# Kernel tuning notes

Hardware: AMD Instinct MI355X
Metric: run time of the kernel (lower is better)

The kernel has to match this reference:

```python
import jax, jax.numpy as jnp
import numpy as np

B, H, S = 128, 256, 19
K0, D0 = 512, 32
K1, D1 = 512, 64
K2, D2 = 512, 64


def _conv(x, w, b):
    # 3x3 SAME conv, NCHW / OIHW
    y = jax.lax.conv_general_dilated(x, w, (1, 1), 'SAME',
                                     dimension_numbers=('NCHW', 'OIHW', 'NCHW'))
    return y + b[None, :, None, None]


def _bn(x, g, b, eps=1e-5):
    # BatchNorm2d in training mode: batch statistics over (N, H, W)
    m = x.mean((0, 2, 3), keepdims=True)
    v = x.var((0, 2, 3), keepdims=True)
    return g[None, :, None, None] * (x - m) * jax.lax.rsqrt(v + eps) + b[None, :, None, None]


def _vq(lat, E):
    # cdist^2 -> argmin -> gather, with straight-through gradient copy
    shp = lat.shape
    d = E.shape[1]
    lp = lat.reshape(-1, d)                                   # row-major flatten, as torch .view
    dist = (lp * lp).sum(-1, keepdims=True) + (E * E).sum(-1) - 2.0 * (lp @ E.T)
    k = jnp.argmin(dist, axis=-1)
    zd = E[k]
    zg = lp + jax.lax.stop_gradient(zd - lp)
    return k.reshape(shp[0], -1), zd.reshape(shp), zg.reshape(shp)


def setup_inputs() -> dict:
    key = jax.random.key(0)
    ks = iter(jax.random.split(key, 64))
    def rn(shape, s=0.02):
        return (s * jax.random.normal(next(ks), shape)).astype(jnp.float32)
    inp = {
        'observations': jax.random.normal(next(ks), (B, 18, S, S), jnp.float32),
        'hierarchy_usages': jax.random.uniform(next(ks), (B, 2), jnp.float32),
        'h0_conv_w': rn((H, 18, 3, 3), 0.05), 'h0_conv_b': jnp.zeros((H,)),
        'h0_bn_g': jnp.ones((H,)), 'h0_bn_b': jnp.zeros((H,)),
        'rb_c1_w': rn((3, H, H, 3, 3)), 'rb_c1_b': jnp.zeros((3, H)),
        'rb_bn1_g': jnp.ones((3, H)), 'rb_bn1_b': jnp.zeros((3, H)),
        'rb_c2_w': rn((3, H, H, 3, 3)), 'rb_c2_b': jnp.zeros((3, H)),
        'rb_bn2_g': jnp.ones((3, H)), 'rb_bn2_b': jnp.zeros((3, H)),
        'h0_conv2_w': rn((32, H, 3, 3)), 'h0_conv2_b': jnp.zeros((32,)),
        'h0_bn2_g': jnp.ones((32,)), 'h0_bn2_b': jnp.zeros((32,)),
        'E0': rn((K0, D0)), 'E1': rn((K1, D1)), 'E2': rn((K2, D2)),
        'h1_fc_w': rn((D0 * S * S, 256)), 'h1_fc_b': jnp.zeros((256,)),
        'h1_fc2_w': rn((256, D1 * 8)), 'h1_fc2_b': jnp.zeros((D1 * 8,)),
        'h2_fc_w': rn((D1 * 8, 128)), 'h2_fc_b': jnp.zeros((128,)),
        'h2_fc2_w': rn((128, D2 * 8)), 'h2_fc2_b': jnp.zeros((D2 * 8,)),
        'h2_fc3_w': rn((D2 * 8, 128)), 'h2_fc3_b': jnp.zeros((128,)),
        'h2_fc4_w': rn((128, D1 * 8)), 'h2_fc4_b': jnp.zeros((D1 * 8,)),
        'h1_fc3_w': rn((D1 * 8, 256)), 'h1_fc3_b': jnp.zeros((256,)),
        'h1_fc4_w': rn((256, D0 * S * S)), 'h1_fc4_b': jnp.zeros((D0 * S * S,)),
        'policy_w': rn((32 * S * S, 362)), 'policy_b': jnp.zeros((362,)),
        'value_w': rn((32 * S * S, 1)), 'value_b': jnp.zeros((1,)),
    }
    return inp


def _forward(observations, hierarchy_usages, h0_conv_w, h0_conv_b, h0_bn_g, h0_bn_b,
             rb_c1_w, rb_c1_b, rb_bn1_g, rb_bn1_b, rb_c2_w, rb_c2_b, rb_bn2_g, rb_bn2_b,
             h0_conv2_w, h0_conv2_b, h0_bn2_g, h0_bn2_b, E0, E1, E2,
             h1_fc_w, h1_fc_b, h1_fc2_w, h1_fc2_b, h2_fc_w, h2_fc_b, h2_fc2_w, h2_fc2_b,
             h2_fc3_w, h2_fc3_b, h2_fc4_w, h2_fc4_b, h1_fc3_w, h1_fc3_b, h1_fc4_w, h1_fc4_b,
             policy_w, policy_b, value_w, value_b):
    n = observations.shape[0]
    x = jax.nn.relu(_bn(_conv(observations, h0_conv_w, h0_conv_b), h0_bn_g, h0_bn_b))
    for i in range(3):
        xi = x
        x = jax.nn.relu(_bn(_conv(x, rb_c1_w[i], rb_c1_b[i]), rb_bn1_g[i], rb_bn1_b[i]))
        x = _bn(_conv(x, rb_c2_w[i], rb_c2_b[i]), rb_bn2_g[i], rb_bn2_b[i])
        x = jax.nn.relu(xi + x)
    x = jnp.tanh(_bn(_conv(x, h0_conv2_w, h0_conv2_b), h0_bn2_g, h0_bn2_b))  # [B,32,19,19]
    ze0 = x
    k0, zq0, zql0 = _vq(x, E0)
    em0 = jnp.broadcast_to(E0.mean(0)[None, :, None, None], (n, E0.shape[1], S, S))
    x = jax.lax.stop_gradient(x).reshape(-1, 32 * S * S)
    x = jax.nn.relu(x @ h1_fc_w + h1_fc_b)
    x = jnp.tanh(x @ h1_fc2_w + h1_fc2_b).reshape(-1, E1.shape[1], 8)
    ze1 = x
    k1, zq1, zql1 = _vq(x, E1)
    em1 = jnp.broadcast_to(E1.mean(0)[None, :, None], (n, E1.shape[1], 8))
    x = jax.lax.stop_gradient(x).reshape(-1, E1.shape[1] * 8)
    x = jax.nn.relu(x @ h2_fc_w + h2_fc_b)
    x = jnp.tanh(x @ h2_fc2_w + h2_fc2_b).reshape(-1, E2.shape[1], 8)
    ze2 = x
    k2, zq2, zql2 = _vq(x, E2)
    em2 = jnp.broadcast_to(E2.mean(0)[None, :, None], (n, E2.shape[1], 8))
    # top-down decoder path
    x = zql2.reshape(-1, E2.shape[1] * 8)
    x = jax.nn.relu(x @ h2_fc3_w + h2_fc3_b)
    x = jnp.tanh(x @ h2_fc4_w + h2_fc4_b).reshape(-1, E1.shape[1], 8)
    u1 = hierarchy_usages[:, 1][:, None, None]
    x = u1 * zql1 + (1.0 - u1) * x
    x = x.reshape(-1, E1.shape[1] * 8)
    x = jax.nn.relu(x @ h1_fc3_w + h1_fc3_b)
    x = jnp.tanh(x @ h1_fc4_w + h1_fc4_b).reshape(-1, E0.shape[1], S, S)
    u0 = hierarchy_usages[:, 0][:, None, None, None]
    x = u0 * zql0 + (1.0 - u0) * x
    x = x.reshape(-1, 32 * S * S)
    policy = x @ policy_w + policy_b
    value = jnp.tanh(x @ value_w + value_b)
    return (policy, value, ze0, ze1, ze2, zq0, zq1, zq2, k0, k1, k2,
            zql0, zql1, zql2, em0, em1, em2)


def reference(observations, hierarchy_usages, h0_conv_w, h0_conv_b, h0_bn_g, h0_bn_b,
              rb_c1_w, rb_c1_b, rb_bn1_g, rb_bn1_b, rb_c2_w, rb_c2_b, rb_bn2_g, rb_bn2_b,
              h0_conv2_w, h0_conv2_b, h0_bn2_g, h0_bn2_b, E0, E1, E2,
              h1_fc_w, h1_fc_b, h1_fc2_w, h1_fc2_b, h2_fc_w, h2_fc_b, h2_fc2_w, h2_fc2_b,
              h2_fc3_w, h2_fc3_b, h2_fc4_w, h2_fc4_b, h1_fc3_w, h1_fc3_b, h1_fc4_w, h1_fc4_b,
              policy_w, policy_b, value_w, value_b):
    return _forward(observations, hierarchy_usages, h0_conv_w, h0_conv_b, h0_bn_g, h0_bn_b,
                    rb_c1_w, rb_c1_b, rb_bn1_g, rb_bn1_b, rb_c2_w, rb_c2_b, rb_bn2_g, rb_bn2_b,
                    h0_conv2_w, h0_conv2_b, h0_bn2_g, h0_bn2_b, E0, E1, E2,
                    h1_fc_w, h1_fc_b, h1_fc2_w, h1_fc2_b, h2_fc_w, h2_fc_b, h2_fc2_w, h2_fc2_b,
                    h2_fc3_w, h2_fc3_b, h2_fc4_w, h2_fc4_b, h1_fc3_w, h1_fc3_b, h1_fc4_w, h1_fc4_b,
                    policy_w, policy_b, value_w, value_b)
```

## Files before the change

### kernel.cpp

```cpp
#include <hip/hip_runtime.h>
#include <hip/hip_bf16.h>

typedef long long i64;
typedef __attribute__((ext_vector_type(8))) short bf16x8;
typedef __attribute__((ext_vector_type(4))) float f32x4;

static constexpr i64 OUT_POLICY = 0;
static constexpr i64 OUT_VALUE  = 46336;
static constexpr i64 OUT_ZE0    = 46464;
static constexpr i64 OUT_ZE1    = 1525120;
static constexpr i64 OUT_ZE2    = 1590656;
static constexpr i64 OUT_ZQ0    = 1656192;
static constexpr i64 OUT_ZQ1    = 3134848;
static constexpr i64 OUT_ZQ2    = 3200384;
static constexpr i64 OUT_K0     = 3265920;
static constexpr i64 OUT_K1     = 3312128;
static constexpr i64 OUT_K2     = 3313152;
static constexpr i64 OUT_ZQL0   = 3314176;
static constexpr i64 OUT_ZQL1   = 4792832;
static constexpr i64 OUT_ZQL2   = 4858368;
static constexpr i64 OUT_EM0    = 4923904;
static constexpr i64 OUT_EM1    = 6402560;
static constexpr i64 OUT_EM2    = 6468096;
static constexpr i64 OUT_TOTAL  = 6533632;

__device__ __forceinline__ short bf16_hi(float v, float* back)
{
    unsigned b = __float_as_uint(v);
    unsigned hb = (b + 0x8000u) & 0xFFFF0000u;
    *back = __uint_as_float(hb);
    return (short)(hb >> 16);
}
__device__ __forceinline__ short bf16_of(float v)
{
    return (short)((__float_as_uint(v) + 0x8000u) >> 16);
}

__global__ void wtr_k(const float* __restrict__ w, float* __restrict__ wt,
                      int COUT, int CIN)
{
    int total = COUT * CIN * 9;
    for (int idx = blockIdx.x * blockDim.x + threadIdx.x; idx < total;
         idx += gridDim.x * blockDim.x) {
        int co = idx / (CIN * 9);
        int r  = idx - co * CIN * 9;
        int ci = r / 9;
        int tap = r - ci * 9;
        wt[((i64)tap * CIN + ci) * COUT + co] = w[idx];
    }
}

__global__ void wtr4_k(const float* __restrict__ w, short* __restrict__ wt4,
                       int CIN, int COUT)
{
    int NC = CIN / 32;
    int total = NC * 9 * 2 * 8192;
    for (int idx = blockIdx.x * blockDim.x + threadIdx.x; idx < total;
         idx += gridDim.x * blockDim.x) {
        int tile = idx >> 13;
        int pos  = idx & 8191;
        int row   = pos >> 6;
        int sslot = (pos >> 3) & 7;
        int r     = pos & 7;
        int slot  = sslot ^ (row & 7);
        int k2    = slot * 8 + r;
        int ct = tile & 1;
        int s  = tile >> 1;
        int c  = s / 9, t = s - c * 9;
        int co = ct * 128 + row;
        int ci = c * 32 + (k2 & 31);
        short outv = 0;
        if (co < COUT) {
            float v = w[((i64)co * CIN + ci) * 9 + t];
            float hf;
            short hs = bf16_hi(v, &hf);
            outv = (k2 < 32) ? hs : bf16_of(v - hf);
        }
        wt4[idx] = outv;
    }
}

template<int CIN>
__global__ __launch_bounds__(256)
void convmfma_k(const float* __restrict__ X, const short* __restrict__ WT4,
                float* __restrict__ Y, int coutT)
{
    constexpr int NC = CIN / 32;
    constexpr int NS = NC * 9;
    __shared__ short At[2][8192];
    __shared__ short Bt[2][8192];
    const int tid  = threadIdx.x;
    const int lane = tid & 63;
    const int w    = tid >> 6;
    const int wco  = (w & 1) * 64;
    const int wsp  = (w >> 1) * 64;
    const int col0 = blockIdx.x * 128;
    const int ct   = blockIdx.y;
    const int co0  = ct * 128;

    const int spS = tid & 127;
    const int cig = tid >> 7;
    const int colS = col0 + spS;
    const int nS = colS / 361;
    const int sS = colS - nS * 361;
    const int yS = sS / 19, xS = sS - yS * 19;
    const float* Xb = X + (i64)nS * CIN * 361 + sS;

    float xvP[16], xvQ[16];

#define BAR16 asm volatile("s_waitcnt vmcnt(16) lgkmcnt(0)\n\ts_barrier" ::: "memory")
#define BAR0  asm volatile("s_waitcnt vmcnt(0) lgkmcnt(0)\n\ts_barrier" ::: "memory")

#define A_ISSUE(BUF, S)                                                         \
    {                                                                           \
        const short* gp0 = WT4 + ((i64)((S) * 2 + ct) << 13) + (w << 11) + (lane << 3); \
        short* lp0 = &At[BUF][(w << 11)];                                       \
        __builtin_amdgcn_global_load_lds(gp0,        lp0,        16, 0, 0);     \
        __builtin_amdgcn_global_load_lds(gp0 + 512,  lp0 + 512,  16, 0, 0);     \
        __builtin_amdgcn_global_load_lds(gp0 + 1024, lp0 + 1024, 16, 0, 0);     \
        __builtin_amdgcn_global_load_lds(gp0 + 1536, lp0 + 1536, 16, 0, 0);     \
    }

#define B_LOAD(S, XV)                                                           \
    {                                                                           \
        const int c_ = (S) / 9, t_ = (S) - c_ * 9;                              \
        const int ky_ = t_ / 3, kx_ = t_ - ky_ * 3;                             \
        const bool v_ = (yS + ky_ >= 1) & (yS + ky_ <= 19) &                    \
                        (xS + kx_ >= 1) & (xS + kx_ <= 19);                     \
        const float* xp_ = Xb + (i64)(c_ * 32 + cig * 16) * 361                 \
                              + (ky_ - 1) * 19 + (kx_ - 1);                     \
        _Pragma("unroll")                                                       \
        for (int j = 0; j < 16; j++) XV[j] = v_ ? xp_[(i64)j * 361] : 0.f;      \
    }

#define B_WRITE(BUF, XV)                                                        \
    {                                                                           \
        bf16x8 h0, h1, l0, l1;                                                  \
        _Pragma("unroll")                                                       \
        for (int j = 0; j < 8; j++) {                                           \
            float hf;                                                           \
            short hs = bf16_hi(XV[j], &hf);                                     \
            h0[j] = hs; l0[j] = bf16_of(XV[j] - hf);                            \
        }                                                                       \
        _Pragma("unroll")                                                       \
        for (int j = 0; j < 8; j++) {                                           \
            float hf;                                                           \
            short hs = bf16_hi(XV[8 + j], &hf);                                 \
            h1[j] = hs; l1[j] = bf16_of(XV[8 + j] - hf);                        \
        }                                                                       \
        short* bp = &Bt[BUF][spS << 6];                                         \
        const int sw = spS & 7;                                                 \
        *(bf16x8*)(bp + (((cig * 2 + 0) ^ sw) << 3)) = h0;                      \
        *(bf16x8*)(bp + (((cig * 2 + 1) ^ sw) << 3)) = h1;                      \
        *(bf16x8*)(bp + (((4 + cig * 2 + 0) ^ sw) << 3)) = l0;                  \
        *(bf16x8*)(bp + (((4 + cig * 2 + 1) ^ sw) << 3)) = l1;                  \
    }

#define COMPUTE(CUR)                                                            \
    {                                                                           \
        bf16x8 bfr[2][4];                                                       \
        _Pragma("unroll")                                                       \
        for (int hb = 0; hb < 2; hb++)                                          \
            _Pragma("unroll")                                                   \
            for (int fb = 0; fb < 4; fb++) {                                    \
                int row = wsp + fb * 16 + (lane & 15);                          \
                int slot = hb * 4 + (lane >> 4);                                \
                bfr[hb][fb] = *(const bf16x8*)&Bt[CUR][(row << 6) + (((slot ^ (row & 7))) << 3)]; \
            }                                                                   \
        _Pragma("unroll")                                                       \
        for (int ha = 0; ha < 2; ha++)                                          \
            _Pragma("unroll")                                                   \
            for (int fa = 0; fa < 4; fa++) {                                    \
                int row = wco + fa * 16 + (lane & 15);                          \
                int slot = ha * 4 + (lane >> 4);                                \
                bf16x8 af = *(const bf16x8*)&At[CUR][(row << 6) + (((slot ^ (row & 7))) << 3)]; \
                _Pragma("unroll")                                               \
                for (int hb = 0; hb < 2; hb++)                                  \
                    _Pragma("unroll")                                           \
                    for (int fb = 0; fb < 4; fb++)                              \
                        acc[fa][fb] = __builtin_amdgcn_mfma_f32_16x16x32_bf16(  \
                            af, bfr[hb][fb], acc[fa][fb], 0, 0, 0);             \
            }                                                                   \
    }

#define ITER(S, XP, XN)                                                         \
    {                                                                           \
        if ((S) + 1 < NS) { BAR16; } else { BAR0; }                             \
        const int cur_ = ((S) & 1);                                             \
        if ((S) + 1 < NS) A_ISSUE(cur_ ^ 1, (S) + 1)                            \
        if ((S) + 2 < NS) B_LOAD((S) + 2, XN)                                   \
        COMPUTE(cur_)                                                           \
        if ((S) + 1 < NS) B_WRITE(cur_ ^ 1, XP)                                 \
    }

    f32x4 acc[4][4];
#pragma unroll
    for (int i = 0; i < 4; i++)
#pragma unroll
        for (int j = 0; j < 4; j++) acc[i][j] = (f32x4){0.f, 0.f, 0.f, 0.f};

    B_LOAD(0, xvP)
    B_WRITE(0, xvP)
    A_ISSUE(0, 0)
    B_LOAD(1, xvP)

    for (int s = 0; s < NS; s += 2) {
        ITER(s, xvP, xvQ)
        ITER(s + 1, xvQ, xvP)
    }
#undef BAR16
#undef BAR0
#undef A_ISSUE
#undef B_LOAD
#undef B_WRITE
#undef COMPUTE
#undef ITER

#pragma unroll
    for (int fb = 0; fb < 4; fb++) {
        int col = col0 + wsp + fb * 16 + (lane & 15);
        int nT = col / 361, sT = col - nT * 361;
        float* yp = Y + ((i64)nT * coutT + co0 + wco) * 361 + sT;
#pragma unroll
        for (int fa = 0; fa < 4; fa++)
#pragma unroll
            for (int r = 0; r < 4; r++) {
                int m = fa * 16 + (lane >> 4) * 4 + r;
                if (co0 + wco + m < coutT) yp[(i64)m * 361] = acc[fa][fb][r];
            }
    }
}

template<int CIN>
__global__ __launch_bounds__(256)
void convgemm_k(const float* __restrict__ X, const float* __restrict__ wt,
                float* __restrict__ Y, int wtW, int coW0, int coutT)
{
    constexpr int NCB = (CIN + 15) / 16;
    constexpr int NS  = 9 * NCB;
    __shared__ float Ws[2][16][128];
    __shared__ float Bs[2][16][128];
    const int tid  = threadIdx.x;
    const int col0 = blockIdx.x * 128;
    const int co0  = blockIdx.y * 128;
    const int tn = tid & 15;
    const int tm = (tid >> 4) & 15;
    const int kkS  = tid >> 5;
    const int cS0  = (tid & 31) * 4;

    int y_[4], x_[4];
    const float* Xb[4];
#pragma unroll
    for (int j = 0; j < 4; j++) {
        int colj = col0 + cS0 + j;
        int nj = colj / 361;
        int sj = colj - nj * 361;
        y_[j] = sj / 19;
        x_[j] = sj - y_[j] * 19;
        Xb[j] = X + ((i64)nj * CIN) * 361 + sj;
    }

    float4 wA, wB, bA, bB;

#define STAGE(S)                                                               \
    {                                                                          \
        const int tap_ = (S) / NCB, cb_ = ((S) % NCB) * 16;                    \
        const int ky_ = tap_ / 3, kx_ = tap_ - ky_ * 3;                        \
        const int doff_ = (ky_ - 1) * 19 + (kx_ - 1);                          \
        const int ci0_ = cb_ + kkS, ci1_ = ci0_ + 8;                           \
        const float* wr_ = wt + ((i64)(tap_ * CIN) + ci0_) * wtW               \
                              + coW0 + co0 + cS0;                              \
        const bool wok_ = (coW0 + co0 + cS0) < wtW;                            \
        wA = (wok_ && ci0_ < CIN) ? *(const float4*)wr_                        \
                                  : float4{0.f, 0.f, 0.f, 0.f};                \
        wB = (wok_ && ci1_ < CIN) ? *(const float4*)(wr_ + (i64)8 * wtW)       \
                                  : float4{0.f, 0.f, 0.f, 0.f};                \
        bool v0_ = (y_[0]+ky_>=1)&(y_[0]+ky_<=19)&(x_[0]+kx_>=1)&(x_[0]+kx_<=19); \
        bool v1_ = (y_[1]+ky_>=1)&(y_[1]+ky_<=19)&(x_[1]+kx_>=1)&(x_[1]+kx_<=19); \
        bool v2_ = (y_[2]+ky_>=1)&(y_[2]+ky_<=19)&(x_[2]+kx_>=1)&(x_[2]+kx_<=19); \
        bool v3_ = (y_[3]+ky_>=1)&(y_[3]+ky_<=19)&(x_[3]+kx_>=1)&(x_[3]+kx_<=19); \
        bA.x = (v0_ && ci0_ < CIN) ? Xb[0][(i64)ci0_ * 361 + doff_] : 0.f;     \
        bA.y = (v1_ && ci0_ < CIN) ? Xb[1][(i64)ci0_ * 361 + doff_] : 0.f;     \
        bA.z = (v2_ && ci0_ < CIN) ? Xb[2][(i64)ci0_ * 361 + doff_] : 0.f;     \
        bA.w = (v3_ && ci0_ < CIN) ? Xb[3][(i64)ci0_ * 361 + doff_] : 0.f;     \
        bB.x = (v0_ && ci1_ < CIN) ? Xb[0][(i64)ci1_ * 361 + doff_] : 0.f;     \
        bB.y = (v1_ && ci1_ < CIN) ? Xb[1][(i64)ci1_ * 361 + doff_] : 0.f;     \
        bB.z = (v2_ && ci1_ < CIN) ? Xb[2][(i64)ci1_ * 361 + doff_] : 0.f;     \
        bB.w = (v3_ && ci1_ < CIN) ? Xb[3][(i64)ci1_ * 361 + doff_] : 0.f;     \
    }

#define WRITE(BUF)                                                             \
    {                                                                          \
        *(float4*)&Ws[BUF][kkS    ][cS0] = wA;                                 \
        *(float4*)&Ws[BUF][kkS + 8][cS0] = wB;                                 \
        *(float4*)&Bs[BUF][kkS    ][cS0] = bA;                                 \
        *(float4*)&Bs[BUF][kkS + 8][cS0] = bB;                                 \
    }

    float acc[8][8];
#pragma unroll
    for (int i = 0; i < 8; i++)
#pragma unroll
        for (int j = 0; j < 8; j++) acc[i][j] = 0.f;

    STAGE(0)
    WRITE(0)
    int cur = 0;
    for (int s = 0; s < NS; s++) {
        __syncthreads();
        if (s + 1 < NS) STAGE(s + 1)
#pragma unroll
        for (int kk = 0; kk < 16; kk++) {
            const float4 w0 = *(const float4*)&Ws[cur][kk][tm * 4];
            const float4 w1 = *(const float4*)&Ws[cur][kk][tm * 4 + 64];
            const float4 b0 = *(const float4*)&Bs[cur][kk][tn * 4];
            const float4 b1 = *(const float4*)&Bs[cur][kk][tn * 4 + 64];
            float wv[8] = {w0.x, w0.y, w0.z, w0.w, w1.x, w1.y, w1.z, w1.w};
            float bv[8] = {b0.x, b0.y, b0.z, b0.w, b1.x, b1.y, b1.z, b1.w};
#pragma unroll
            for (int wi = 0; wi < 8; wi++)
#pragma unroll
                for (int bj = 0; bj < 8; bj++)
                    acc[wi][bj] = fmaf(wv[wi], bv[bj], acc[wi][bj]);
        }
        if (s + 1 < NS) WRITE(cur ^ 1)
        cur ^= 1;
    }
#undef STAGE
#undef WRITE

#pragma unroll
    for (int bj = 0; bj < 8; bj++) {
        int lc = (bj < 4) ? (tn * 4 + bj) : (64 + tn * 4 + bj - 4);
        int colT = col0 + lc;
        int nT = colT / 361;
        int sT = colT - nT * 361;
        float* yp = Y + ((i64)nT * coutT + co0) * 361 + sT;
#pragma unroll
        for (int wi = 0; wi < 8; wi++) {
            int co = (wi < 4) ? (tm * 4 + wi) : (64 + tm * 4 + wi - 4);
            if (co0 + co < coutT) yp[(i64)co * 361] = acc[wi][bj];
        }
    }
}

__global__ __launch_bounds__(256)
void bnstats_k(const float* __restrict__ x, const float* __restrict__ g,
               const float* __restrict__ b, float* __restrict__ scale,
               float* __restrict__ shift, int C)
{
    const int c = blockIdx.x;
    float s = 0.f, s2 = 0.f;
    for (int n = 0; n < 128; n++) {
        const float* p = x + ((i64)n * C + c) * 361;
        for (int i = threadIdx.x; i < 361; i += 256) {
            float v = p[i]; s += v; s2 += v * v;
        }
    }
    __shared__ float rs[4], rq[4];
    for (int o = 32; o > 0; o >>= 1) { s += __shfl_down(s, o); s2 += __shfl_down(s2, o); }
    int lane = threadIdx.x & 63, wid = threadIdx.x >> 6;
    if (lane == 0) { rs[wid] = s; rq[wid] = s2; }
    __syncthreads();
    if (threadIdx.x == 0) {
        float S = rs[0] + rs[1] + rs[2] + rs[3];
        float Q = rq[0] + rq[1] + rq[2] + rq[3];
        const float inv = 1.f / 46208.f;
        float m  = S * inv;
        float var = Q * inv - m * m;
        float sc = g[c] * rsqrtf(var + 1e-5f);
        scale[c] = sc;
        shift[c] = b[c] - m * sc;
    }
}

__global__ void bn_relu4_k(float4* __restrict__ x, const float* __restrict__ scale,
                           const float* __restrict__ shift, int C, int total4)
{
    for (int i = blockIdx.x * blockDim.x + threadIdx.x; i < total4; i += gridDim.x * blockDim.x) {
        float4 v = x[i];
        int e = i * 4;
        int c0 = (e / 361) % C, c1 = ((e + 1) / 361) % C;
        int c2 = ((e + 2) / 361) % C, c3 = ((e + 3) / 361) % C;
        v.x = fmaf(v.x, scale[c0], shift[c0]); v.x = v.x > 0.f ? v.x : 0.f;
        v.y = fmaf(v.y, scale[c1], shift[c1]); v.y = v.y > 0.f ? v.y : 0.f;
        v.z = fmaf(v.z, scale[c2], shift[c2]); v.z = v.z > 0.f ? v.z : 0.f;
        v.w = fmaf(v.w, scale[c3], shift[c3]); v.w = v.w > 0.f ? v.w : 0.f;
        x[i] = v;
    }
}

__global__ void bn_add_relu4_k(float4* __restrict__ xa, const float4* __restrict__ xc,
                               const float* __restrict__ scale, const float* __restrict__ shift,
                               int C, int total4)
{
    for (int i = blockIdx.x * blockDim.x + threadIdx.x; i < total4; i += gridDim.x * blockDim.x) {
        float4 a = xa[i], c = xc[i];
        int e = i * 4;
        int c0 = (e / 361) % C, c1 = ((e + 1) / 361) % C;
        int c2 = ((e + 2) / 361) % C, c3 = ((e + 3) / 361) % C;
        a.x += fmaf(c.x, scale[c0], shift[c0]); a.x = a.x > 0.f ? a.x : 0.f;
        a.y += fmaf(c.y, scale[c1], shift[c1]); a.y = a.y > 0.f ? a.y : 0.f;
        a.z += fmaf(c.z, scale[c2], shift[c2]); a.z = a.z > 0.f ? a.z : 0.f;
        a.w += fmaf(c.w, scale[c3], shift[c3]); a.w = a.w > 0.f ? a.w : 0.f;
        xa[i] = a;
    }
}

__global__ void bn_tanh_ws_k(const float* __restrict__ x, const float* __restrict__ scale,
                             const float* __restrict__ shift, float* __restrict__ zf, int total)
{
    for (int i = blockIdx.x * blockDim.x + threadIdx.x; i < total; i += gridDim.x * blockDim.x) {
        int c = (i / 361) & 31;
        zf[i] = tanhf(fmaf(x[i], scale[c], shift[c]));
    }
}

__global__ void prep_k(const float* __restrict__ E0, const float* __restrict__ E1,
                       const float* __restrict__ E2,
                       float* __restrict__ ee0, float* __restrict__ ee1, float* __restrict__ ee2,
                       float* __restrict__ cm0, float* __restrict__ cm1, float* __restrict__ cm2)
{
    int t = threadIdx.x;
    if (blockIdx.x == 0) {
        float s = 0.f; const float* e = E0 + (i64)t * 32;
        for (int d = 0; d < 32; d++) s += e[d] * e[d];
        ee0[t] = s;
    } else if (blockIdx.x == 1) {
        float s = 0.f; const float* e = E1 + (i64)t * 64;
        for (int d = 0; d < 64; d++) s += e[d] * e[d];
        ee1[t] = s;
    } else if (blockIdx.x == 2) {
        float s = 0.f; const float* e = E2 + (i64)t * 64;
        for (int d = 0; d < 64; d++) s += e[d] * e[d];
        ee2[t] = s;
    } else {
        if (t < 32) {
            float s = 0.f; for (int k = 0; k < 512; k++) s += E0[k * 32 + t];
            cm0[t] = s * (1.f / 512.f);
        } else if (t >= 64 && t < 128) {
            int d = t - 64; float s = 0.f; for (int k = 0; k < 512; k++) s += E1[k * 64 + d];
            cm1[d] = s * (1.f / 512.f);
        } else if (t >= 128 && t < 192) {
            int d = t - 128; float s = 0.f; for (int k = 0; k < 512; k++) s += E2[k * 64 + d];
            cm2[d] = s * (1.f / 512.f);
        }
    }
}

__global__ __launch_bounds__(256)
void vq0_k(const float* __restrict__ z, const float* __restrict__ E,
           const float* __restrict__ ee, float* __restrict__ zqf, int* __restrict__ ki)
{
    __shared__ float Es[256 * 32];
    int row = blockIdx.x * 256 + threadIdx.x;
    const bool live = row < 46208;
    const float* zp = z + (i64)(live ? row : 0) * 32;
    float zv[32]; float zz = 0.f;
#pragma unroll
    for (int d = 0; d < 32; d++) { float v = zp[d]; zv[d] = v; zz += v * v; }
    float best = 3.4e38f; int bk = 0;
    for (int h = 0; h < 2; h++) {
        __syncthreads();
        for (int i = threadIdx.x; i < 256 * 32; i += 256) Es[i] = E[h * 8192 + i];
        __syncthreads();
        for (int k = 0; k < 256; k++) {
            const float* e = Es + k * 32;
            float dot = 0.f;
#pragma unroll
            for (int d = 0; d < 32; d++) dot = fmaf(zv[d], e[d], dot);
            float dist = (zz + ee[h * 256 + k]) - 2.f * dot;
            if (dist < best) { best = dist; bk = h * 256 + k; }
        }
    }
    if (live) {
        ki[row] = bk;
        const float* eb = E + (i64)bk * 32;
#pragma unroll
        for (int d = 0; d < 32; d++) zqf[(i64)row * 32 + d] = eb[d];
    }
}

__global__ __launch_bounds__(256)
void vq64_k(const float* __restrict__ z, const float* __restrict__ E,
            const float* __restrict__ ee, float* __restrict__ zqf, int* __restrict__ ki)
{
    __shared__ float Es[128 * 64];
    int row = blockIdx.x * 256 + threadIdx.x;
    const float* zp = z + (i64)row * 64;
    float zv[64]; float zz = 0.f;
#pragma unroll
    for (int d = 0; d < 64; d++) { float v = zp[d]; zv[d] = v; zz += v * v; }
    float best = 3.4e38f; int bk = 0;
    for (int h = 0; h < 4; h++) {
        __syncthreads();
        for (int i = threadIdx.x; i < 128 * 64; i += 256) Es[i] = E[(i64)h * 8192 + i];
        __syncthreads();
        for (int k = 0; k < 128; k++) {
            const float* e = Es + k * 64;
            float dot = 0.f;
#pragma unroll
            for (int d = 0; d < 64; d++) dot = fmaf(zv[d], e[d], dot);
            float dist = (zz + ee[h * 128 + k]) - 2.f * dot;
            if (dist < best) { best = dist; bk = h * 128 + k; }
        }
    }
    ki[row] = bk;
    const float* eb = E + (i64)bk * 64;
#pragma unroll
    for (int d = 0; d < 64; d++) zqf[(i64)row * 64 + d] = eb[d];
}

__global__ __launch_bounds__(256)
void gemm_part_k(const float* __restrict__ A, const float* __restrict__ W,
                 float* __restrict__ part, int K, int N, int kchunk)
{
    __shared__ float As[128][17];
    __shared__ float Ws[16][64];
    const int n0 = blockIdx.x * 64;
    const int ks = blockIdx.y;
    const int kb0  = ks * kchunk;
    const int kend = min(K, kb0 + kchunk);
    const int tid = threadIdx.x;
    const int tn = tid & 15, tm = tid >> 4;
    float acc[8][4];
#pragma unroll
    for (int i = 0; i < 8; i++)
#pragma unroll
        for (int j = 0; j < 4; j++) acc[i][j] = 0.f;

    for (int kb = kb0; kb < kend; kb += 16) {
        __syncthreads();
        for (int i = tid; i < 2048; i += 256) {
            int m = i >> 4, kk = i & 15;
            int k = kb + kk;
            As[m][kk] = (k < kend) ? A[(i64)m * K + k] : 0.f;
        }
        for (int i = tid; i < 1024; i += 256) {
            int kk = i >> 6, nl = i & 63;
            int k = kb + kk, n = n0 + nl;
            Ws[kk][nl] = (k < kend && n < N) ? W[(i64)k * N + n] : 0.f;
        }
        __syncthreads();
#pragma unroll
        for (int kk = 0; kk < 16; kk++) {
            float av[8], wv[4];
#pragma unroll
            for (int i = 0; i < 8; i++) av[i] = As[tm * 8 + i][kk];
#pragma unroll
            for (int j = 0; j < 4; j++) wv[j] = Ws[kk][tn * 4 + j];
#pragma unroll
            for (int i = 0; i < 8; i++)
#pragma unroll
                for (int j = 0; j < 4; j++) acc[i][j] = fmaf(av[i], wv[j], acc[i][j]);
        }
    }
#pragma unroll
    for (int i = 0; i < 8; i++) {
        int m = tm * 8 + i;
#pragma unroll
        for (int j = 0; j < 4; j++) {
            int n = n0 + tn * 4 + j;
            if (n < N) part[((i64)ks * 128 + m) * N + n] = acc[i][j];
        }
    }
}

__global__ void combine_k(const float* __restrict__ part, const float* __restrict__ bias,
                          float* __restrict__ of, int MN, int N, int ksplit, int act)
{
    for (int i = blockIdx.x * blockDim.x + threadIdx.x; i < MN; i += gridDim.x * blockDim.x) {
        float s = 0.f;
        for (int t = 0; t < ksplit; t++) s += part[(i64)t * MN + i];
        s += bias[i % N];
        if (act == 1) s = s > 0.f ? s : 0.f;
        else if (act == 2) s = tanhf(s);
        of[i] = s;
    }
}

__global__ void blend_k(const float* __restrict__ q, const float* __restrict__ d,
                        const float* __restrict__ hu, int col, float* __restrict__ o,
                        int per_b, int total)
{
    for (int i = blockIdx.x * blockDim.x + threadIdx.x; i < total; i += gridDim.x * blockDim.x) {
        float u = hu[(i / per_b) * 2 + col];
        o[i] = u * q[i] + (1.f - u) * d[i];
    }
}

__global__ __launch_bounds__(256)
void value_k(const float* __restrict__ x, const float* __restrict__ w,
             const float* __restrict__ b, float* __restrict__ valf)
{
    int m = blockIdx.x;
    float s = 0.f;
    const float* xp = x + (i64)m * 11552;
    for (int k = threadIdx.x; k < 11552; k += 256) s = fmaf(xp[k], w[k], s);
    for (int o = 32; o > 0; o >>= 1) s += __shfl_down(s, o);
    __shared__ float r[4];
    int lane = threadIdx.x & 63, wid = threadIdx.x >> 6;
    if (lane == 0) r[wid] = s;
    __syncthreads();
    if (threadIdx.x == 0)
        valf[m] = tanhf(r[0] + r[1] + r[2] + r[3] + b[0]);
}

__global__ void emit_f32_k(const float* __restrict__ src, float* __restrict__ out, i64 off, int n)
{
    for (int i = blockIdx.x * blockDim.x + threadIdx.x; i < n; i += gridDim.x * blockDim.x)
        out[off + i] = src[i];
}

__global__ void emit_dup_k(const float* __restrict__ src, float* __restrict__ out,
                           i64 off1, i64 off2, int n)
{
    for (int i = blockIdx.x * blockDim.x + threadIdx.x; i < n; i += gridDim.x * blockDim.x) {
        float v = src[i];
        out[off1 + i] = v;
        out[off2 + i] = v;
    }
}

__global__ void emit_k_k(const int* __restrict__ ki, float* __restrict__ out, i64 off, int n)
{
    for (int i = blockIdx.x * blockDim.x + threadIdx.x; i < n; i += gridDim.x * blockDim.x)
        out[off + i] = (float)ki[i];
}

__global__ void emit_em_k(const float* __restrict__ cm, float* __restrict__ out, i64 off,
                          int D, int SPL, int total)
{
    for (int i = blockIdx.x * blockDim.x + threadIdx.x; i < total; i += gridDim.x * blockDim.x) {
        int c = (i / SPL) % D;
        out[off + i] = cm[c];
    }
}

__global__ void marker_k(float* __restrict__ out, int code)
{
    if (threadIdx.x < 64) out[threadIdx.x] = 3000.f + 100.f * code;
}

__global__ void sentinel_k(float* __restrict__ out)
{
    if (threadIdx.x < 128) out[OUT_VALUE + threadIdx.x] = 2000.0f;
}

extern "C" void kernel_launch(void* const* d_in, const int* in_sizes, int n_in,
                              void* d_out, int out_size, void* d_ws, size_t ws_size,
                              hipStream_t stream)
{
    float* out = (float*)d_out;

    int bad = -1;
    if (out_size != (int)OUT_TOTAL) bad = 0;
    else if (n_in != 41) bad = 1;
    else if (in_sizes[0] != 128 * 18 * 361) bad = 2;
    else if (in_sizes[21] != 11552 * 256) bad = 3;
    if (bad >= 0) { marker_k<<<1, 64, 0, stream>>>(out, bad); return; }

    const float* obs   = (const float*)d_in[0];
    const float* hier  = (const float*)d_in[1];
    const float* c0w   = (const float*)d_in[2];
    const float* bn0g  = (const float*)d_in[4];
    const float* bn0b  = (const float*)d_in[5];
    const float* rb1w  = (const float*)d_in[6];
    const float* rbn1g = (const float*)d_in[8];
    const float* rbn1b = (const float*)d_in[9];
    const float* rb2w  = (const float*)d_in[10];
    const float* rbn2g = (const float*)d_in[12];
    const float* rbn2b = (const float*)d_in[13];
    const float* c2w   = (const float*)d_in[14];
    const float* bn2g  = (const float*)d_in[16];
    const float* bn2b  = (const float*)d_in[17];
    const float* E0    = (const float*)d_in[18];
    const float* E1    = (const float*)d_in[19];
    const float* E2    = (const float*)d_in[20];
    const float* fc1w  = (const float*)d_in[21]; const float* fc1b  = (const float*)d_in[22];
    const float* fc2w  = (const float*)d_in[23]; const float* fc2b  = (const float*)d_in[24];
    const float* h2fw  = (const float*)d_in[25]; const float* h2fb  = (const float*)d_in[26];
    const float* h2f2w = (const float*)d_in[27]; const float* h2f2b = (const float*)d_in[28];
    const float* h2f3w = (const float*)d_in[29]; const float* h2f3b = (const float*)d_in[30];
    const float* h2f4w = (const float*)d_in[31]; const float* h2f4b = (const float*)d_in[32];
    const float* h1f3w = (const float*)d_in[33]; const float* h1f3b = (const float*)d_in[34];
    const float* h1f4w = (const float*)d_in[35]; const float* h1f4b = (const float*)d_in[36];
    const float* polw  = (const float*)d_in[37]; const float* polb  = (const float*)d_in[38];
    const float* valw  = (const float*)d_in[39]; const float* valb  = (const float*)d_in[40];

    float* wsf = (float*)d_ws;

    const size_t NEED_A = (size_t)36732928 * 4;
    const size_t NEED_C = (size_t)27860992 * 4;
    if (ws_size < NEED_C) {
        sentinel_k<<<1, 128, 0, stream>>>(out);
        return;
    }
    const bool fullC = (ws_size >= NEED_A);

    float* scale = wsf + 0;        float* shift = wsf + 256;
    float* ee0 = wsf + 512;        float* ee1 = wsf + 1024;   float* ee2 = wsf + 1536;
    float* cm0 = wsf + 2048;       float* cm1 = wsf + 2112;   float* cm2 = wsf + 2176;
    int*   k0i = (int*)(wsf + 4096);
    int*   k1i = (int*)(wsf + 50304);
    int*   k2i = (int*)(wsf + 51328);
    float* h1a  = wsf + 53248;
    float* ze1f = wsf + 86016;
    float* zq1f = wsf + 151552;
    float* h2a  = wsf + 217088;
    float* ze2f = wsf + 233472;
    float* zq2f = wsf + 299008;
    float* h2b  = wsf + 364544;
    float* decf = wsf + 380928;
    float* x1f  = wsf + 446464;
    float* h1b  = wsf + 512000;
    float* polf = wsf + 544768;
    float* valf = wsf + 591104;

    float* A    = wsf + 655360;
    float* B    = wsf + 12484608;
    float* C    = wsf + 24313856;
    float* WT   = fullC ? (wsf + 36143104) : (wsf + 27271168);
    float* ze0f = A;
    float* zq0f = wsf + 655360 + 1572864;
    float* dec0 = wsf + 655360 + 3145728;
    float* xf   = wsf + 655360 + 4718592;
    float* part = B;

    short* WT4 = (short*)d_out;

    const int TOT256 = 128 * 256 * 361;
    const int TOT32  = 128 * 32 * 361;
    const int TOT64  = 128 * 64 * 361;

    prep_k<<<4, 512, 0, stream>>>(E0, E1, E2, ee0, ee1, ee2, cm0, cm1, cm2);

    wtr_k<<<64, 256, 0, stream>>>(c0w, WT, 256, 18);
    convgemm_k<18><<<dim3(361, 2), 256, 0, stream>>>(obs, WT, A, 256, 0, 256);
    bnstats_k<<<256, 256, 0, stream>>>(A, bn0g, bn0b, scale, shift, 256);
    bn_relu4_k<<<1024, 256, 0, stream>>>((float4*)A, scale, shift, 256, TOT256 / 4);

    for (int i = 0; i < 3; i++) {
        if (fullC) {
            wtr4_k<<<1024, 256, 0, stream>>>(rb1w + (i64)i * 589824, WT4, 256, 256);
            convmfma_k<256><<<dim3(361, 2), 256, 0, stream>>>(A, WT4, B, 256);
        } else {
            wtr_k<<<576, 256, 0, stream>>>(rb1w + (i64)i * 589824, WT, 256, 256);
            convgemm_k<256><<<dim3(361, 2), 256, 0, stream>>>(A, WT, B, 256, 0, 256);
        }
        bnstats_k<<<256, 256, 0, stream>>>(B, rbn1g + i * 256, rbn1b + i * 256, scale, shift, 256);
        bn_relu4_k<<<1024, 256, 0, stream>>>((float4*)B, scale, shift, 256, TOT256 / 4);
        if (fullC) {
            wtr4_k<<<1024, 256, 0, stream>>>(rb2w + (i64)i * 589824, WT4, 256, 256);
            convmfma_k<256><<<dim3(361, 2), 256, 0, stream>>>(B, WT4, C, 256);
            bnstats_k<<<256, 256, 0, stream>>>(C, rbn2g + i * 256, rbn2b + i * 256, scale, shift, 256);
            bn_add_relu4_k<<<1024, 256, 0, stream>>>((float4*)A, (const float4*)C, scale, shift, 256, TOT256 / 4);
        } else {
            wtr_k<<<576, 256, 0, stream>>>(rb2w + (i64)i * 589824, WT, 256, 256);
            convgemm_k<256><<<dim3(361, 2), 256, 0, stream>>>(B, WT, C, 256, 0, 256);
            bnstats_k<<<256, 256, 0, stream>>>(C, rbn2g + i * 256, rbn2b + i * 256, scale, shift, 256);
            bn_add_relu4_k<<<1024, 256, 0, stream>>>((float4*)A, (const float4*)C, scale, shift, 256, TOT256 / 4);
        }
    }

    if (fullC) {
        wtr4_k<<<1024, 256, 0, stream>>>(c2w, WT4, 256, 32);
        convmfma_k<256><<<dim3(361, 1), 256, 0, stream>>>(A, WT4, C, 32);
    } else {
        wtr_k<<<72, 256, 0, stream>>>(c2w, WT, 32, 256);
        convgemm_k<256><<<dim3(361, 1), 256, 0, stream>>>(A, WT, C, 32, 0, 32);
    }
    bnstats_k<<<32, 256, 0, stream>>>(C, bn2g, bn2b, scale, shift, 32);
    bn_tanh_ws_k<<<1024, 256, 0, stream>>>(C, scale, shift, ze0f, TOT32);

    vq0_k<<<181, 256, 0, stream>>>(ze0f, E0, ee0, zq0f, k0i);

    gemm_part_k<<<dim3(4, 32), 256, 0, stream>>>(ze0f, fc1w, part, 11552, 256, 361);
    combine_k<<<128, 256, 0, stream>>>(part, fc1b, h1a, 128 * 256, 256, 32, 1);
    gemm_part_k<<<dim3(8, 4), 256, 0, stream>>>(h1a, fc2w, part, 256, 512, 64);
    combine_k<<<256, 256, 0, stream>>>(part, fc2b, ze1f, 128 * 512, 512, 4, 2);
    vq64_k<<<4, 256, 0, stream>>>(ze1f, E1, ee1, zq1f, k1i);

    gemm_part_k<<<dim3(2, 8), 256, 0, stream>>>(ze1f, h2fw, part, 512, 128, 64);
    combine_k<<<64, 256, 0, stream>>>(part, h2fb, h2a, 128 * 128, 128, 8, 1);
    gemm_part_k<<<dim3(8, 2), 256, 0, stream>>>(h2a, h2f2w, part, 128, 512, 64);
    combine_k<<<256, 256, 0, stream>>>(part, h2f2b, ze2f, 128 * 512, 512, 2, 2);
    vq64_k<<<4, 256, 0, stream>>>(ze2f, E2, ee2, zq2f, k2i);

    gemm_part_k<<<dim3(2, 8), 256, 0, stream>>>(zq2f, h2f3w, part, 512, 128, 64);
    combine_k<<<64, 256, 0, stream>>>(part, h2f3b, h2b, 128 * 128, 128, 8, 1);
    gemm_part_k<<<dim3(8, 2), 256, 0, stream>>>(h2b, h2f4w, part, 128, 512, 64);
    combine_k<<<256, 256, 0, stream>>>(part, h2f4b, decf, 128 * 512, 512, 2, 2);
    blend_k<<<256, 256, 0, stream>>>(zq1f, decf, hier, 1, x1f, 512, 65536);

    gemm_part_k<<<dim3(4, 8), 256, 0, stream>>>(x1f, h1f3w, part, 512, 256, 64);
    combine_k<<<128, 256, 0, stream>>>(part, h1f3b, h1b, 128 * 256, 256, 8, 1);
    gemm_part_k<<<dim3(181, 2), 256, 0, stream>>>(h1b, h1f4w, part, 256, 11552, 128);
    combine_k<<<1024, 256, 0, stream>>>(part, h1f4b, dec0, TOT32, 11552, 2, 2);
    blend_k<<<1024, 256, 0, stream>>>(zq0f, dec0, hier, 0, xf, 11552, TOT32);

    gemm_part_k<<<dim3(6, 16), 256, 0, stream>>>(xf, polw, part, 11552, 362, 722);
    combine_k<<<256, 256, 0, stream>>>(part, polb, polf, 128 * 362, 362, 16, 0);
    value_k<<<128, 256, 0, stream>>>(xf, valw, valb, valf);

    emit_f32_k<<<128, 256, 0, stream>>>(polf, out, OUT_POLICY, 46336);
    emit_f32_k<<<1, 128, 0, stream>>>(valf, out, OUT_VALUE, 128);
    emit_f32_k<<<1024, 256, 0, stream>>>(ze0f, out, OUT_ZE0, TOT32);
    emit_f32_k<<<256, 256, 0, stream>>>(ze1f, out, OUT_ZE1, 65536);
    emit_f32_k<<<256, 256, 0, stream>>>(ze2f, out, OUT_ZE2, 65536);
    emit_dup_k<<<1024, 256, 0, stream>>>(zq0f, out, OUT_ZQ0, OUT_ZQL0, TOT32);
    emit_dup_k<<<256, 256, 0, stream>>>(zq1f, out, OUT_ZQ1, OUT_ZQL1, 65536);
    emit_dup_k<<<256, 256, 0, stream>>>(zq2f, out, OUT_ZQ2, OUT_ZQL2, 65536);
    emit_k_k<<<181, 256, 0, stream>>>(k0i, out, OUT_K0, 46208);
    emit_k_k<<<4, 256, 0, stream>>>(k1i, out, OUT_K1, 1024);
    emit_k_k<<<4, 256, 0, stream>>>(k2i, out, OUT_K2, 1024);
    emit_em_k<<<1024, 256, 0, stream>>>(cm0, out, OUT_EM0, 32, 361, TOT32);
    emit_em_k<<<256, 256, 0, stream>>>(cm1, out, OUT_EM1, 64, 8, 65536);
    emit_em_k<<<256, 256, 0, stream>>>(cm2, out, OUT_EM2, 64, 8, 65536);
}
```

Before: 3.592 ms.

## Load conv weight fragments directly into registers and remap blocks across XCDs

The MFMA conv kernel no longer stages the weight tile through LDS with global_load_lds. Each wave now prefetches its A fragments straight from global memory into registers (double-buffered afA/afB), which halves LDS use. The pipeline drops from a two-step lookahead with custom waitcnt barriers to a simpler one-step scheme using __syncthreads. Block indices are also remapped so that contiguous column tiles land on the same XCD for L2 locality. The trade is more register pressure and redundant global weight reads per wave, since waves sharing co rows each reload them.

```diff
diff --git a/kernel.cpp b/kernel.cpp
--- a/kernel.cpp
+++ b/kernel.cpp
@@ -87,14 +87,20 @@
 {
     constexpr int NC = CIN / 32;
     constexpr int NS = NC * 9;
-    __shared__ short At[2][8192];
     __shared__ short Bt[2][8192];
     const int tid  = threadIdx.x;
     const int lane = tid & 63;
     const int w    = tid >> 6;
     const int wco  = (w & 1) * 64;
     const int wsp  = (w >> 1) * 64;
-    const int col0 = blockIdx.x * 128;
+
+    const int q8 = (int)gridDim.x >> 3;
+    const int r8 = (int)gridDim.x & 7;
+    const int xcd = (int)blockIdx.x & 7;
+    const int boff = (int)blockIdx.x >> 3;
+    const int bcol = (xcd < r8) ? (xcd * (q8 + 1) + boff)
+                                : (r8 * (q8 + 1) + (xcd - r8) * q8 + boff);
+    const int col0 = bcol * 128;
     const int ct   = blockIdx.y;
     const int co0  = ct * 128;
 
@@ -106,22 +112,9 @@
     const int yS = sS / 19, xS = sS - yS * 19;
     const float* Xb = X + (i64)nS * CIN * 361 + sS;
 
-    float xvP[16], xvQ[16];
-
-#define BAR16 asm volatile("s_waitcnt vmcnt(16) lgkmcnt(0)\n\ts_barrier" ::: "memory")
-#define BAR0  asm volatile("s_waitcnt vmcnt(0) lgkmcnt(0)\n\ts_barrier" ::: "memory")
-
-#define A_ISSUE(BUF, S)                                                         \
-    {                                                                           \
-        const short* gp0 = WT4 + ((i64)((S) * 2 + ct) << 13) + (w << 11) + (lane << 3); \
-        short* lp0 = &At[BUF][(w << 11)];                                       \
-        __builtin_amdgcn_global_load_lds(gp0,        lp0,        16, 0, 0);     \
-        __builtin_amdgcn_global_load_lds(gp0 + 512,  lp0 + 512,  16, 0, 0);     \
-        __builtin_amdgcn_global_load_lds(gp0 + 1024, lp0 + 1024, 16, 0, 0);     \
-        __builtin_amdgcn_global_load_lds(gp0 + 1536, lp0 + 1536, 16, 0, 0);     \
-    }
-
-#define B_LOAD(S, XV)                                                           \
+    float xv[16];
+
+#define B_LOAD(S)                                                               \
     {                                                                           \
         const int c_ = (S) / 9, t_ = (S) - c_ * 9;                              \
         const int ky_ = t_ / 3, kx_ = t_ - ky_ * 3;                             \
@@ -130,23 +123,23 @@
         const float* xp_ = Xb + (i64)(c_ * 32 + cig * 16) * 361                 \
                               + (ky_ - 1) * 19 + (kx_ - 1);                     \
         _Pragma("unroll")                                                       \
-        for (int j = 0; j < 16; j++) XV[j] = v_ ? xp_[(i64)j * 361] : 0.f;      \
-    }
-
-#define B_WRITE(BUF, XV)                                                        \
+        for (int j = 0; j < 16; j++) xv[j] = v_ ? xp_[(i64)j * 361] : 0.f;      \
+    }
+
+#define B_WRITE(BUF)                                                            \
     {                                                                           \
         bf16x8 h0, h1, l0, l1;                                                  \
         _Pragma("unroll")                                                       \
         for (int j = 0; j < 8; j++) {                                           \
             float hf;                                                           \
-            short hs = bf16_hi(XV[j], &hf);                                     \
-            h0[j] = hs; l0[j] = bf16_of(XV[j] - hf);                            \
+            short hs = bf16_hi(xv[j], &hf);                                     \
+            h0[j] = hs; l0[j] = bf16_of(xv[j] - hf);                            \
         }                                                                       \
         _Pragma("unroll")                                                       \
         for (int j = 0; j < 8; j++) {                                           \
             float hf;                                                           \
-            short hs = bf16_hi(XV[8 + j], &hf);                                 \
-            h1[j] = hs; l1[j] = bf16_of(XV[8 + j] - hf);                        \
+            short hs = bf16_hi(xv[8 + j], &hf);                                 \
+            h1[j] = hs; l1[j] = bf16_of(xv[8 + j] - hf);                        \
         }                                                                       \
         short* bp = &Bt[BUF][spS << 6];                                         \
         const int sw = spS & 7;                                                 \
@@ -156,7 +149,20 @@
         *(bf16x8*)(bp + (((4 + cig * 2 + 1) ^ sw) << 3)) = l1;                  \
     }
 
-#define COMPUTE(CUR)                                                            \
+#define A_PREF(AFR, S)                                                          \
+    {                                                                           \
+        const short* tb_ = WT4 + ((i64)((S) * 2 + ct) << 13);                   \
+        _Pragma("unroll")                                                       \
+        for (int ha = 0; ha < 2; ha++)                                          \
+            _Pragma("unroll")                                                   \
+            for (int fa = 0; fa < 4; fa++) {                                    \
+                int row = wco + fa * 16 + (lane & 15);                          \
+                int slot = ha * 4 + (lane >> 4);                                \
+                AFR[ha][fa] = *(const bf16x8*)(tb_ + (row << 6) + (((slot ^ (row & 7))) << 3)); \
+            }                                                                   \
+    }
+
+#define COMPUTE(CUR, AFR)                                                       \
     {                                                                           \
         bf16x8 bfr[2][4];                                                       \
         _Pragma("unroll")                                                       \
@@ -171,9 +177,7 @@
         for (int ha = 0; ha < 2; ha++)                                          \
             _Pragma("unroll")                                                   \
             for (int fa = 0; fa < 4; fa++) {                                    \
-                int row = wco + fa * 16 + (lane & 15);                          \
-                int slot = ha * 4 + (lane >> 4);                                \
-                bf16x8 af = *(const bf16x8*)&At[CUR][(row << 6) + (((slot ^ (row & 7))) << 3)]; \
+                bf16x8 af = AFR[ha][fa];                                        \
                 _Pragma("unroll")                                               \
                 for (int hb = 0; hb < 2; hb++)                                  \
                     _Pragma("unroll")                                           \
@@ -183,38 +187,36 @@
             }                                                                   \
     }
 
-#define ITER(S, XP, XN)                                                         \
-    {                                                                           \
-        if ((S) + 1 < NS) { BAR16; } else { BAR0; }                             \
-        const int cur_ = ((S) & 1);                                             \
-        if ((S) + 1 < NS) A_ISSUE(cur_ ^ 1, (S) + 1)                            \
-        if ((S) + 2 < NS) B_LOAD((S) + 2, XN)                                   \
-        COMPUTE(cur_)                                                           \
-        if ((S) + 1 < NS) B_WRITE(cur_ ^ 1, XP)                                 \
-    }
-
     f32x4 acc[4][4];
 #pragma unroll
     for (int i = 0; i < 4; i++)
 #pragma unroll
         for (int j = 0; j < 4; j++) acc[i][j] = (f32x4){0.f, 0.f, 0.f, 0.f};
 
-    B_LOAD(0, xvP)
-    B_WRITE(0, xvP)
-    A_ISSUE(0, 0)
-    B_LOAD(1, xvP)
+    bf16x8 afA[2][4], afB[2][4];
+
+    B_LOAD(0)
+    B_WRITE(0)
+    A_PREF(afA, 0)
 
     for (int s = 0; s < NS; s += 2) {
-        ITER(s, xvP, xvQ)
-        ITER(s + 1, xvQ, xvP)
-    }
-#undef BAR16
-#undef BAR0
-#undef A_ISSUE
+        __syncthreads();
+        B_LOAD(s + 1)
+        A_PREF(afB, s + 1)
+        COMPUTE(0, afA)
+        B_WRITE(1)
+        __syncthreads();
+        if (s + 2 < NS) {
+            B_LOAD(s + 2)
+            A_PREF(afA, s + 2)
+        }
+        COMPUTE(1, afB)
+        if (s + 2 < NS) B_WRITE(0)
+    }
 #undef B_LOAD
 #undef B_WRITE
+#undef A_PREF
 #undef COMPUTE
-#undef ITER
 
 #pragma unroll
     for (int fb = 0; fb < 4; fb++) {
@@ -696,7 +698,7 @@
         sentinel_k<<<1, 128, 0, stream>>>(out);
         return;
     }
-    const bool fullC = (ws_size >= NEED_A);
+    const bool mfma = (ws_size >= NEED_A);
 
     float* scale = wsf + 0;        float* shift = wsf + 256;
     float* ee0 = wsf + 512;        float* ee1 = wsf + 1024;   float* ee2 = wsf + 1536;
@@ -717,21 +719,20 @@
     float* polf = wsf + 544768;
     float* valf = wsf + 591104;
 
-    float* A    = wsf + 655360;
-    float* B    = wsf + 12484608;
-    float* C    = wsf + 24313856;
-    float* WT   = fullC ? (wsf + 36143104) : (wsf + 27271168);
+    float* A   = wsf + 655360;
+    float* R   = wsf + 12484608;
+    float* C   = wsf + 24313856;
+    float* WT  = mfma ? (wsf + 36143104) : (wsf + 27271168);
     float* ze0f = A;
     float* zq0f = wsf + 655360 + 1572864;
     float* dec0 = wsf + 655360 + 3145728;
     float* xf   = wsf + 655360 + 4718592;
-    float* part = B;
+    float* part = R;
 
     short* WT4 = (short*)d_out;
 
     const int TOT256 = 128 * 256 * 361;
     const int TOT32  = 128 * 32 * 361;
-    const int TOT64  = 128 * 64 * 361;
 
     prep_k<<<4, 512, 0, stream>>>(E0, E1, E2, ee0, ee1, ee2, cm0, cm1, cm2);
 
@@ -740,38 +741,37 @@
     bnstats_k<<<256, 256, 0, stream>>>(A, bn0g, bn0b, scale, shift, 256);
     bn_relu4_k<<<1024, 256, 0, stream>>>((float4*)A, scale, shift, 256, TOT256 / 4);
 
-    for (int i = 0; i < 3; i++) {
-        if (fullC) {
+    if (mfma) {
+        for (int i = 0; i < 3; i++) {
             wtr4_k<<<1024, 256, 0, stream>>>(rb1w + (i64)i * 589824, WT4, 256, 256);
-            convmfma_k<256><<<dim3(361, 2), 256, 0, stream>>>(A, WT4, B, 256);
-        } else {
-            wtr_k<<<576, 256, 0, stream>>>(rb1w + (i64)i * 589824, WT, 256, 256);
-            convgemm_k<256><<<dim3(361, 2), 256, 0, stream>>>(A, WT, B, 256, 0, 256);
-        }
-        bnstats_k<<<256, 256, 0, stream>>>(B, rbn1g + i * 256, rbn1b + i * 256, scale, shift, 256);
-        bn_relu4_k<<<1024, 256, 0, stream>>>((float4*)B, scale, shift, 256, TOT256 / 4);
-        if (fullC) {
+            convmfma_k<256><<<dim3(361, 2), 256, 0, stream>>>(A, WT4, R, 256);
+            bnstats_k<<<256, 256, 0, stream>>>(R, rbn1g + i * 256, rbn1b + i * 256, scale, shift, 256);
+            bn_relu4_k<<<1024, 256, 0, stream>>>((float4*)R, scale, shift, 256, TOT256 / 4);
             wtr4_k<<<1024, 256, 0, stream>>>(rb2w + (i64)i * 589824, WT4, 256, 256);
-            convmfma_k<256><<<dim3(361, 2), 256, 0, stream>>>(B, WT4, C, 256);
+            convmfma_k<256><<<dim3(361, 2), 256, 0, stream>>>(R, WT4, C, 256);
             bnstats_k<<<256, 256, 0, stream>>>(C, rbn2g + i * 256, rbn2b + i * 256, scale, shift, 256);
             bn_add_relu4_k<<<1024, 256, 0, stream>>>((float4*)A, (const float4*)C, scale, shift, 256, TOT256 / 4);
-        } else {
+        }
+        wtr4_k<<<1024, 256, 0, stream>>>(c2w, WT4, 256, 32);
+        convmfma_k<256><<<dim3(361, 1), 256, 0, stream>>>(A, WT4, C, 32);
+        bnstats_k<<<32, 256, 0, stream>>>(C, bn2g, bn2b, scale, shift, 32);
+        bn_tanh_ws_k<<<1024, 256, 0, stream>>>(C, scale, shift, ze0f, TOT32);
+    } else {
+        for (int i = 0; i < 3; i++) {
+            wtr_k<<<576, 256, 0, stream>>>(rb1w + (i64)i * 589824, WT, 256, 256);
+            convgemm_k<256><<<dim3(361, 2), 256, 0, stream>>>(A, WT, R, 256, 0, 256);
+            bnstats_k<<<256, 256, 0, stream>>>(R, rbn1g + i * 256, rbn1b + i * 256, scale, shift, 256);
+            bn_relu4_k<<<1024, 256, 0, stream>>>((float4*)R, scale, shift, 256, TOT256 / 4);
             wtr_k<<<576, 256, 0, stream>>>(rb2w + (i64)i * 589824, WT, 256, 256);
-            convgemm_k<256><<<dim3(361, 2), 256, 0, stream>>>(B, WT, C, 256, 0, 256);
+            convgemm_k<256><<<dim3(361, 2), 256, 0, stream>>>(R, WT, C, 256, 0, 256);
             bnstats_k<<<256, 256, 0, stream>>>(C, rbn2g + i * 256, rbn2b + i * 256, scale, shift, 256);
             bn_add_relu4_k<<<1024, 256, 0, stream>>>((float4*)A, (const float4*)C, scale, shift, 256, TOT256 / 4);
         }
-    }
-
-    if (fullC) {
-        wtr4_k<<<1024, 256, 0, stream>>>(c2w, WT4, 256, 32);
-        convmfma_k<256><<<dim3(361, 1), 256, 0, stream>>>(A, WT4, C, 32);
-    } else {
         wtr_k<<<72, 256, 0, stream>>>(c2w, WT, 32, 256);
         convgemm_k<256><<<dim3(361, 1), 256, 0, stream>>>(A, WT, C, 32, 0, 32);
-    }
-    bnstats_k<<<32, 256, 0, stream>>>(C, bn2g, bn2b, scale, shift, 32);
-    bn_tanh_ws_k<<<1024, 256, 0, stream>>>(C, scale, shift, ze0f, TOT32);
+        bnstats_k<<<32, 256, 0, stream>>>(C, bn2g, bn2b, scale, shift, 32);
+        bn_tanh_ws_k<<<1024, 256, 0, stream>>>(C, scale, shift, ze0f, TOT32);
+    }
 
     vq0_k<<<181, 256, 0, stream>>>(ze0f, E0, ee0, zq0f, k0i);
 
```

Result: slower. 3.997 ms (+11.3%).
